# Kernel tuning notes

Measured on AMD Instinct MI355X. Metric: run time of the kernel, lower is better.

Reference implementation:

```python
import jax, jax.numpy as jnp
import numpy as np

N_NODES = 50000
N_EDGES = 800000
IN_DIM = 128
HID = 128
N_GRAPHS = 256
N_CLASSES = 2
ALPHA = 0.2  # leaky relu slope
EPS_BN = 1e-5


def setup_inputs() -> dict:
    key = jax.random.key(0)
    ks = jax.random.split(key, 24)
    adjacency = jax.random.randint(ks[0], (2, N_EDGES), 0, N_NODES, dtype=jnp.int32)
    input_feature = jax.random.normal(ks[1], (N_NODES, IN_DIM), dtype=jnp.float32)
    graph_indicator = jnp.sort(jax.random.randint(ks[2], (N_NODES,), 0, N_GRAPHS, dtype=jnp.int32))
    labels = jax.random.randint(ks[3], (N_GRAPHS,), 0, N_CLASSES, dtype=jnp.int64)
    s = 0.05
    params = {
        'W1': jax.random.normal(ks[4], (IN_DIM, HID), jnp.float32) * s,
        'a1': jax.random.normal(ks[5], (2 * HID,), jnp.float32) * s,
        'bn2_g': jnp.ones((HID,), jnp.float32),
        'bn2_b': jnp.zeros((HID,), jnp.float32),
        'W2': jax.random.normal(ks[6], (HID, HID), jnp.float32) * s,
        'a2': jax.random.normal(ks[7], (2 * HID,), jnp.float32) * s,
        'bn3_g': jnp.ones((HID,), jnp.float32),
        'bn3_b': jnp.zeros((HID,), jnp.float32),
        'W3': jax.random.normal(ks[8], (HID, HID), jnp.float32) * s,
        'a3': jax.random.normal(ks[9], (2 * HID,), jnp.float32) * s,
        'fc1_w': jax.random.normal(ks[10], (HID, 2 * HID), jnp.float32) * s,
        'fc1_b': jnp.zeros((2 * HID,), jnp.float32),
        'fc2_w': jax.random.normal(ks[11], (2 * HID, HID), jnp.float32) * s,
        'fc2_b': jnp.zeros((HID,), jnp.float32),
        'fc3_w': jax.random.normal(ks[12], (HID, N_CLASSES), jnp.float32) * s,
        'fc3_b': jnp.zeros((N_CLASSES,), jnp.float32),
    }
    return dict(adjacency=adjacency, input_feature=input_feature,
                graph_indicator=graph_indicator, labels=labels, **params)


def _batchnorm(x, g, b):
    # training-mode BatchNorm1d over node dim (biased variance)
    mu = jnp.mean(x, axis=0)
    var = jnp.mean((x - mu) ** 2, axis=0)
    return (x - mu) * jax.lax.rsqrt(var + EPS_BN) * g + b


def _sp_gat(x, src, dst, W, a):
    # pyGAT SpGraphAttentionLayer (dropout disabled / eval mode)
    h = x @ W                                # [N, F]
    F = h.shape[1]
    e_src = h @ a[:F]                        # [N]
    e_dst = h @ a[F:]                        # [N]
    e = e_src[src] + e_dst[dst]              # [E]
    ee = jnp.exp(-jax.nn.leaky_relu(e, ALPHA))
    rowsum = jax.ops.segment_sum(ee, src, num_segments=N_NODES)          # [N]
    num = jax.ops.segment_sum(ee[:, None] * h[dst], src, num_segments=N_NODES)  # [N, F]
    h_prime = num / (rowsum[:, None] + 1e-16)
    return jax.nn.elu(h_prime)


def reference(adjacency, input_feature, graph_indicator, labels,
              W1, a1, bn2_g, bn2_b, W2, a2, bn3_g, bn3_b, W3, a3,
              fc1_w, fc1_b, fc2_w, fc2_b, fc3_w, fc3_b):
    src, dst = adjacency[0], adjacency[1]
    # bn1 output is discarded in the original forward
    x = _sp_gat(input_feature, src, dst, W1, a1)
    x = _batchnorm(x, bn2_g, bn2_b)
    x = _sp_gat(x, src, dst, W2, a2)
    x = _batchnorm(x, bn3_g, bn3_b)
    x = _sp_gat(x, src, dst, W3, a3)
    # pooling_sum_4tensor: per-graph sum pooling
    pooled = jax.ops.segment_sum(x, graph_indicator, num_segments=N_GRAPHS)  # [G, F]
    x = jax.nn.relu(pooled @ fc1_w + fc1_b)
    x = jax.nn.relu(x @ fc2_w + fc2_b)
    logits = x @ fc3_w + fc3_b
    return logits
```

## Files before the change

kernel.cpp:

```cpp
#include <hip/hip_runtime.h>
#include <hip/hip_bf16.h>

#define N_NODES 50000
#define N_EDGES 800000
#define FD 128
#define N_GRAPHS 256
#define NPART 6250

typedef unsigned short u16;
typedef short bf16x8 __attribute__((ext_vector_type(8)));
typedef float f32x4 __attribute__((ext_vector_type(4)));

__device__ __forceinline__ u16 f2bf(float v) {
    __hip_bfloat16 h = __float2bfloat16(v);
    union { __hip_bfloat16 hh; u16 u; } c; c.hh = h; return c.u;
}
__device__ __forceinline__ float bf2f(u16 r) {
    return __uint_as_float(((unsigned int)r) << 16);
}

__global__ __launch_bounds__(256) void count_deg_part_k(const int* __restrict__ src,
                                                        int* __restrict__ cnt, int E) {
    int part = blockIdx.x & 7;
    int lo = part * NPART, hi = lo + NPART;
    int stride = (gridDim.x >> 3) * 256;
    for (int e = (blockIdx.x >> 3) * 256 + threadIdx.x; e < E; e += stride) {
        int s = src[e];
        if (s >= lo && s < hi) atomicAdd(&cnt[s], 1);
    }
}

__global__ __launch_bounds__(256) void fill_csr_part_k(const int* __restrict__ src,
                                                       const int* __restrict__ dst,
                                                       int* __restrict__ cur,
                                                       int* __restrict__ edst, int E) {
    int part = blockIdx.x & 7;
    int lo = part * NPART, hi = lo + NPART;
    int stride = (gridDim.x >> 3) * 256;
    for (int e = (blockIdx.x >> 3) * 256 + threadIdx.x; e < E; e += stride) {
        int s = src[e];
        if (s >= lo && s < hi) {
            int p = atomicAdd(&cur[s], 1);
            edst[p] = dst[e];
        }
    }
}

__global__ __launch_bounds__(256) void scan1_k(const int* __restrict__ cnt,
                                               int* __restrict__ bsum, int M,
                                               float* __restrict__ bnbuf,
                                               float* __restrict__ pooled) {
    int i = blockIdx.x * 256 + threadIdx.x;
    int v = (i < M) ? cnt[i] : 0;
    __shared__ int l[256];
    l[threadIdx.x] = v;
    __syncthreads();
    for (int s = 128; s > 0; s >>= 1) {
        if (threadIdx.x < s) l[threadIdx.x] += l[threadIdx.x + s];
        __syncthreads();
    }
    if (threadIdx.x == 0) bsum[blockIdx.x] = l[0];
    if (blockIdx.x == 0) {
        bnbuf[threadIdx.x] = 0.f; bnbuf[threadIdx.x + 256] = 0.f;
        for (int k = threadIdx.x; k < N_GRAPHS * FD; k += 256) pooled[k] = 0.f;
    }
}

__global__ __launch_bounds__(256) void scan3_k(const int* __restrict__ cnt,
                                               const int* __restrict__ bsum,
                                               int* __restrict__ offs,
                                               int* __restrict__ cur, int M, int NB) {
    int i = blockIdx.x * 256 + threadIdx.x;
    int tid = threadIdx.x;
    __shared__ int bs[256];
    bs[tid] = (tid < NB) ? bsum[tid] : 0;
    __syncthreads();
    for (int off = 1; off < 256; off <<= 1) {
        int t = (tid >= off) ? bs[tid - off] : 0;
        __syncthreads();
        bs[tid] += t;
        __syncthreads();
    }
    int base = (blockIdx.x == 0) ? 0 : bs[blockIdx.x - 1];
    int v = (i < M) ? cnt[i] : 0;
    __shared__ int l[256];
    l[tid] = v;
    __syncthreads();
    for (int off = 1; off < 256; off <<= 1) {
        int t = (tid >= off) ? l[tid - off] : 0;
        __syncthreads();
        l[tid] += t;
        __syncthreads();
    }
    int excl = l[tid] - v + base;
    if (i < M) { offs[i] = excl; cur[i] = excl; }
    if (i == M - 1) offs[M] = excl + v;
}

__global__ __launch_bounds__(128) void wprep1_k(const float* __restrict__ W,
                                                u16* __restrict__ Wt,
                                                float* __restrict__ cvec) {
    int n = blockIdx.x, k = threadIdx.x;
    Wt[(size_t)n * FD + k] = f2bf(W[(size_t)k * FD + n]);
    if (k == 0) cvec[n] = 0.f;
}

__global__ __launch_bounds__(128) void bnfw_k(const float* __restrict__ W,
                                              const float* __restrict__ sums,
                                              const float* __restrict__ sumsq,
                                              const float* __restrict__ g,
                                              const float* __restrict__ b,
                                              float invN,
                                              u16* __restrict__ Wt,
                                              float* __restrict__ cvec) {
    int n = blockIdx.x, k = threadIdx.x;
    __shared__ float scs[128], shs[128], l[128];
    float mu = sums[k] * invN;
    float var = sumsq[k] * invN - mu * mu;
    float sc = g[k] * rsqrtf(var + 1e-5f);
    scs[k] = sc;
    shs[k] = b[k] - mu * sc;
    __syncthreads();
    float w = W[(size_t)k * FD + n];
    Wt[(size_t)n * FD + k] = f2bf(scs[k] * w);
    l[k] = shs[k] * w;
    __syncthreads();
    for (int s = 64; s > 0; s >>= 1) {
        if (k < s) l[k] += l[k + s];
        __syncthreads();
    }
    if (k == 0) cvec[n] = l[0];
}

__global__ __launch_bounds__(256) void gemm_mfma_k(const float* __restrict__ Xf,
                                                   const u16* __restrict__ Xb,
                                                   int use_f32,
                                                   const u16* __restrict__ Wt,
                                                   const float* __restrict__ cvec,
                                                   const float* __restrict__ avec,
                                                   u16* __restrict__ Hb,
                                                   float* __restrict__ es,
                                                   float* __restrict__ ed, int M) {
    __shared__ u16 As[64][136];
    __shared__ u16 Bs[128][136];
    __shared__ float sa_s[128], sa_d[128], cv[128];
    int tid = threadIdx.x;
    if (tid < 128) { sa_s[tid] = avec[tid]; sa_d[tid] = avec[128 + tid]; cv[tid] = cvec[tid]; }
    int row0 = blockIdx.x * 64;
    {
        int n = tid >> 1, k0 = (tid & 1) * 64;
        const uint4* s = (const uint4*)(Wt + (size_t)n * FD + k0);
#pragma unroll
        for (int u = 0; u < 8; u++) *(uint4*)&Bs[n][k0 + u * 8] = s[u];
    }
    {
        int r = tid >> 2, k0 = (tid & 3) * 32;
        int grow = row0 + r;
        if (grow < M) {
            if (use_f32) {
                const float4* s = (const float4*)(Xf + (size_t)grow * FD + k0);
#pragma unroll
                for (int u = 0; u < 8; u++) {
                    float4 v = s[u];
                    ushort4 o;
                    o.x = f2bf(v.x); o.y = f2bf(v.y); o.z = f2bf(v.z); o.w = f2bf(v.w);
                    *(ushort4*)&As[r][k0 + u * 4] = o;
                }
            } else {
                const uint4* s = (const uint4*)(Xb + (size_t)grow * FD + k0);
#pragma unroll
                for (int u = 0; u < 4; u++) *(uint4*)&As[r][k0 + u * 8] = s[u];
            }
        } else {
            uint4 z = make_uint4(0, 0, 0, 0);
#pragma unroll
            for (int u = 0; u < 4; u++) *(uint4*)&As[r][k0 + u * 8] = z;
        }
    }
    __syncthreads();

    int wave = tid >> 6, lane = tid & 63;
    int quad = lane >> 4, n16 = lane & 15;
    int rbase = wave * 16;
    f32x4 acc[8];
    f32x4 zz = {0.f, 0.f, 0.f, 0.f};
#pragma unroll
    for (int t = 0; t < 8; t++) acc[t] = zz;

#pragma unroll
    for (int kk = 0; kk < 128; kk += 32) {
        bf16x8 a = *(const bf16x8*)&As[rbase + n16][kk + quad * 8];
#pragma unroll
        for (int t = 0; t < 8; t++) {
            bf16x8 b = *(const bf16x8*)&Bs[t * 16 + n16][kk + quad * 8];
            acc[t] = __builtin_amdgcn_mfma_f32_16x16x32_bf16(a, b, acc[t], 0, 0, 0);
        }
    }

#pragma unroll
    for (int reg = 0; reg < 4; reg++) {
        int grow = row0 + rbase + quad * 4 + reg;
        float vals[8];
        float ps = 0.f, pd = 0.f;
#pragma unroll
        for (int t = 0; t < 8; t++) {
            float v = acc[t][reg] + cv[t * 16 + n16];
            vals[t] = v;
            ps += v * sa_s[t * 16 + n16];
            pd += v * sa_d[t * 16 + n16];
        }
#pragma unroll
        for (int o = 8; o > 0; o >>= 1) { ps += __shfl_xor(ps, o); pd += __shfl_xor(pd, o); }
        if (grow < M) {
            if (n16 == 0) { es[grow] = ps; ed[grow] = pd; }
#pragma unroll
            for (int t = 0; t < 8; t++)
                Hb[(size_t)grow * FD + t * 16 + n16] = f2bf(vals[t]);
        }
    }
}

__global__ __launch_bounds__(256) void agg_k(const u16* __restrict__ Hb,
                                             const float* __restrict__ es_,
                                             const float* __restrict__ ed_,
                                             const int* __restrict__ offs,
                                             const int* __restrict__ edst,
                                             u16* __restrict__ Out, int M) {
    int node = __builtin_amdgcn_readfirstlane((int)((blockIdx.x * blockDim.x + threadIdx.x) >> 6));
    int lane = threadIdx.x & 63;
    if (node >= M) return;
    int s0 = offs[node], s1 = offs[node + 1];
    float esv = es_[node];
    const unsigned int* Hrow = (const unsigned int*)Hb;
    float2 a0 = make_float2(0.f, 0.f), a1 = make_float2(0.f, 0.f);
    float2 a2 = make_float2(0.f, 0.f), a3 = make_float2(0.f, 0.f);
    float rs = 0.f;
    int e = s0;
    for (; e + 8 <= s1; e += 8) {
        int d[8];
#pragma unroll
        for (int u = 0; u < 8; u++) d[u] = __builtin_amdgcn_readfirstlane(edst[e + u]);
        float w[8];
#pragma unroll
        for (int u = 0; u < 8; u++) {
            float ev = esv + ed_[d[u]];
            float lr = ev > 0.f ? ev : 0.2f * ev;
            w[u] = __expf(-lr);
        }
        unsigned int r[8];
#pragma unroll
        for (int u = 0; u < 8; u++) r[u] = Hrow[(size_t)d[u] * 64 + lane];
#pragma unroll
        for (int u = 0; u < 8; u++) {
            rs += w[u];
            float2* ac = (u & 3) == 0 ? &a0 : (u & 3) == 1 ? &a1 : (u & 3) == 2 ? &a2 : &a3;
            ac->x += w[u] * __int_as_float(r[u] << 16);
            ac->y += w[u] * __int_as_float(r[u] & 0xffff0000u);
        }
    }
    for (; e < s1; e++) {
        int d = __builtin_amdgcn_readfirstlane(edst[e]);
        float ev = esv + ed_[d];
        float lr = ev > 0.f ? ev : 0.2f * ev;
        float wv = __expf(-lr);
        rs += wv;
        unsigned int r = Hrow[(size_t)d * 64 + lane];
        a0.x += wv * __int_as_float(r << 16);
        a0.y += wv * __int_as_float(r & 0xffff0000u);
    }
    float inv = 1.f / (rs + 1e-16f);
    float vx = (a0.x + a1.x + a2.x + a3.x) * inv;
    float vy = (a0.y + a1.y + a2.y + a3.y) * inv;
    vx = vx > 0.f ? vx : (__expf(vx) - 1.f);
    vy = vy > 0.f ? vy : (__expf(vy) - 1.f);
    unsigned int pk = ((unsigned int)f2bf(vy) << 16) | f2bf(vx);
    ((unsigned int*)Out)[(size_t)node * 64 + lane] = pk;
}

__global__ void bnstats_b_k(const u16* __restrict__ Xb, float* __restrict__ sums,
                            float* __restrict__ sumsq, int M) {
    int f = threadIdx.x & 127;
    int half = threadIdx.x >> 7;
    float s1 = 0.f, s2 = 0.f;
    for (int r = blockIdx.x * 2 + half; r < M; r += gridDim.x * 2) {
        float v = bf2f(Xb[(size_t)r * FD + f]);
        s1 += v; s2 += v * v;
    }
    __shared__ float l1[256], l2[256];
    l1[threadIdx.x] = s1; l2[threadIdx.x] = s2;
    __syncthreads();
    if (half == 0) {
        atomicAdd(&sums[f], l1[f] + l1[f + 128]);
        atomicAdd(&sumsq[f], l2[f] + l2[f + 128]);
    }
}

__global__ void pool_k(const u16* __restrict__ Xb, const int* __restrict__ gi,
                       float* __restrict__ pooled, int M) {
    int f = threadIdx.x & 127;
    int half = threadIdx.x >> 7;
    int r0 = blockIdx.x * 128 + half;
    int rend = min(blockIdx.x * 128 + 128, M);
    int curg = -1; float acc = 0.f;
    for (int r = r0; r < rend; r += 2) {
        int g = gi[r];
        if (g != curg) {
            if (curg >= 0) atomicAdd(&pooled[(size_t)curg * FD + f], acc);
            curg = g; acc = 0.f;
        }
        acc += bf2f(Xb[(size_t)r * FD + f]);
    }
    if (curg >= 0) atomicAdd(&pooled[(size_t)curg * FD + f], acc);
}

__global__ __launch_bounds__(256) void mlp_k(const float* __restrict__ pooled,
                                             const float* __restrict__ fc1w, const float* __restrict__ fc1b,
                                             const float* __restrict__ fc2w, const float* __restrict__ fc2b,
                                             const float* __restrict__ fc3w, const float* __restrict__ fc3b,
                                             float* __restrict__ out) {
    int g = blockIdx.x, j = threadIdx.x;
    __shared__ float x[128], t1[256], t2[128], p0[128], p1[128];
    if (j < 128) x[j] = pooled[(size_t)g * FD + j];
    __syncthreads();
    float s = fc1b[j];
    for (int k = 0; k < 128; k++) s += x[k] * fc1w[(size_t)k * 256 + j];
    t1[j] = fmaxf(s, 0.f);
    __syncthreads();
    if (j < 128) {
        float s2 = fc2b[j];
        for (int k = 0; k < 256; k++) s2 += t1[k] * fc2w[(size_t)k * 128 + j];
        t2[j] = fmaxf(s2, 0.f);
    }
    __syncthreads();
    if (j < 128) { p0[j] = t2[j] * fc3w[j * 2]; p1[j] = t2[j] * fc3w[j * 2 + 1]; }
    __syncthreads();
    for (int s3 = 64; s3 > 0; s3 >>= 1) {
        if (j < s3) { p0[j] += p0[j + s3]; p1[j] += p1[j + s3]; }
        __syncthreads();
    }
    if (j == 0) { out[g * 2] = p0[0] + fc3b[0]; out[g * 2 + 1] = p1[0] + fc3b[1]; }
}

extern "C" void kernel_launch(void* const* d_in, const int* in_sizes, int n_in,
                              void* d_out, int out_size, void* d_ws, size_t ws_size,
                              hipStream_t stream) {
    const int*   adj  = (const int*)d_in[0];
    const float* xin  = (const float*)d_in[1];
    const int*   gi   = (const int*)d_in[2];
    const float* W1   = (const float*)d_in[4];
    const float* a1   = (const float*)d_in[5];
    const float* bn2g = (const float*)d_in[6];
    const float* bn2b = (const float*)d_in[7];
    const float* W2   = (const float*)d_in[8];
    const float* a2   = (const float*)d_in[9];
    const float* bn3g = (const float*)d_in[10];
    const float* bn3b = (const float*)d_in[11];
    const float* W3   = (const float*)d_in[12];
    const float* a3   = (const float*)d_in[13];
    const float* fc1w = (const float*)d_in[14];
    const float* fc1b = (const float*)d_in[15];
    const float* fc2w = (const float*)d_in[16];
    const float* fc2b = (const float*)d_in[17];
    const float* fc3w = (const float*)d_in[18];
    const float* fc3b = (const float*)d_in[19];
    float* out = (float*)d_out;

    const int N = N_NODES, E = N_EDGES, G = N_GRAPHS;

    u16*   Xb     = (u16*)d_ws;
    u16*   Hb     = Xb + (size_t)N * FD;
    u16*   Wt     = Hb + (size_t)N * FD;
    float* es     = (float*)(Wt + FD * FD);
    float* ed     = es + N;
    float* bnbuf  = ed + N;
    float* sumsA  = bnbuf;
    float* sumsqA = bnbuf + 128;
    float* sumsB  = bnbuf + 256;
    float* sumsqB = bnbuf + 384;
    float* cvec   = bnbuf + 512;
    float* pooled = cvec + FD;
    int*   degcnt = (int*)(pooled + (size_t)G * FD);
    int*   offs   = degcnt + N;
    int*   cur    = offs + (N + 2);
    int*   bsum   = cur + N;
    int*   edst   = bsum + 256;

    const int* srcp = adj;
    const int* dstp = adj + E;

    const int NB = (N + 255) / 256;

    hipMemsetAsync(degcnt, 0, (size_t)N * sizeof(int), stream);
    count_deg_part_k<<<8 * 392, 256, 0, stream>>>(srcp, degcnt, E);
    scan1_k<<<NB, 256, 0, stream>>>(degcnt, bsum, N, bnbuf, pooled);
    scan3_k<<<NB, 256, 0, stream>>>(degcnt, bsum, offs, cur, N, NB);
    fill_csr_part_k<<<8 * 392, 256, 0, stream>>>(srcp, dstp, cur, edst, E);

    const int gemm_grid = (N + 63) / 64;
    const int wave_grid = (N + 3) / 4;
    const float invN = 1.0f / (float)N;

    wprep1_k<<<FD, 128, 0, stream>>>(W1, Wt, cvec);
    gemm_mfma_k<<<gemm_grid, 256, 0, stream>>>(xin, Xb, 1, Wt, cvec, a1, Hb, es, ed, N);
    agg_k<<<wave_grid, 256, 0, stream>>>(Hb, es, ed, offs, edst, Xb, N);
    bnstats_b_k<<<256, 256, 0, stream>>>(Xb, sumsA, sumsqA, N);

    bnfw_k<<<FD, 128, 0, stream>>>(W2, sumsA, sumsqA, bn2g, bn2b, invN, Wt, cvec);
    gemm_mfma_k<<<gemm_grid, 256, 0, stream>>>(nullptr, Xb, 0, Wt, cvec, a2, Hb, es, ed, N);
    agg_k<<<wave_grid, 256, 0, stream>>>(Hb, es, ed, offs, edst, Xb, N);
    bnstats_b_k<<<256, 256, 0, stream>>>(Xb, sumsB, sumsqB, N);

    bnfw_k<<<FD, 128, 0, stream>>>(W3, sumsB, sumsqB, bn3g, bn3b, invN, Wt, cvec);
    gemm_mfma_k<<<gemm_grid, 256, 0, stream>>>(nullptr, Xb, 0, Wt, cvec, a3, Hb, es, ed, N);
    agg_k<<<wave_grid, 256, 0, stream>>>(Hb, es, ed, offs, edst, Xb, N);

    pool_k<<<(N + 127) / 128, 256, 0, stream>>>(Xb, gi, pooled, N);
    mlp_k<<<G, 256, 0, stream>>>(pooled, fc1w, fc1b, fc2w, fc2b, fc3w, fc3b, out);
}
```

Baseline: 428.1 us.

## Split aggregation wavefront into four edge groups with 16-byte row gathers

The per-node aggregation wavefront now splits its 64 lanes into four groups of 16. Each group gathers a different neighbor's bf16 row using 16-byte loads, so each memory instruction covers four edges instead of one. The four partial sums are combined with cross-lane shuffles before the ELU and a 16-byte store by a single group. This aims to raise memory-level parallelism and cut the instruction count of the gather, at the cost of shuffle reductions, more registers, and wasted lanes on padded tail edges.

```diff
diff --git a/kernel.cpp b/kernel.cpp
--- a/kernel.cpp
+++ b/kernel.cpp
@@ -220,6 +220,21 @@
     }
 }
 
+__device__ __forceinline__ void gat4(const uint4* __restrict__ Hq, int p, int g,
+                                     const int* d4, const float* w4, float* acc) {
+    int dg = (g & 2) ? ((g & 1) ? d4[3] : d4[2]) : ((g & 1) ? d4[1] : d4[0]);
+    float wg = (g & 2) ? ((g & 1) ? w4[3] : w4[2]) : ((g & 1) ? w4[1] : w4[0]);
+    uint4 r = Hq[(size_t)dg * 16 + p];
+    acc[0] += wg * __uint_as_float(r.x << 16);
+    acc[1] += wg * __uint_as_float(r.x & 0xffff0000u);
+    acc[2] += wg * __uint_as_float(r.y << 16);
+    acc[3] += wg * __uint_as_float(r.y & 0xffff0000u);
+    acc[4] += wg * __uint_as_float(r.z << 16);
+    acc[5] += wg * __uint_as_float(r.z & 0xffff0000u);
+    acc[6] += wg * __uint_as_float(r.w << 16);
+    acc[7] += wg * __uint_as_float(r.w & 0xffff0000u);
+}
+
 __global__ __launch_bounds__(256) void agg_k(const u16* __restrict__ Hb,
                                              const float* __restrict__ es_,
                                              const float* __restrict__ ed_,
@@ -229,52 +244,62 @@
     int node = __builtin_amdgcn_readfirstlane((int)((blockIdx.x * blockDim.x + threadIdx.x) >> 6));
     int lane = threadIdx.x & 63;
     if (node >= M) return;
+    int g = lane >> 4;
+    int p = lane & 15;
     int s0 = offs[node], s1 = offs[node + 1];
     float esv = es_[node];
-    const unsigned int* Hrow = (const unsigned int*)Hb;
-    float2 a0 = make_float2(0.f, 0.f), a1 = make_float2(0.f, 0.f);
-    float2 a2 = make_float2(0.f, 0.f), a3 = make_float2(0.f, 0.f);
+    const uint4* Hq = (const uint4*)Hb;
+    float acc[8] = {0.f, 0.f, 0.f, 0.f, 0.f, 0.f, 0.f, 0.f};
     float rs = 0.f;
     int e = s0;
     for (; e + 8 <= s1; e += 8) {
-        int d[8];
+        int d[8]; float w[8];
 #pragma unroll
         for (int u = 0; u < 8; u++) d[u] = __builtin_amdgcn_readfirstlane(edst[e + u]);
-        float w[8];
 #pragma unroll
         for (int u = 0; u < 8; u++) {
             float ev = esv + ed_[d[u]];
             float lr = ev > 0.f ? ev : 0.2f * ev;
             w[u] = __expf(-lr);
-        }
-        unsigned int r[8];
-#pragma unroll
-        for (int u = 0; u < 8; u++) r[u] = Hrow[(size_t)d[u] * 64 + lane];
-#pragma unroll
-        for (int u = 0; u < 8; u++) {
             rs += w[u];
-            float2* ac = (u & 3) == 0 ? &a0 : (u & 3) == 1 ? &a1 : (u & 3) == 2 ? &a2 : &a3;
-            ac->x += w[u] * __int_as_float(r[u] << 16);
-            ac->y += w[u] * __int_as_float(r[u] & 0xffff0000u);
-        }
-    }
-    for (; e < s1; e++) {
-        int d = __builtin_amdgcn_readfirstlane(edst[e]);
-        float ev = esv + ed_[d];
-        float lr = ev > 0.f ? ev : 0.2f * ev;
-        float wv = __expf(-lr);
-        rs += wv;
-        unsigned int r = Hrow[(size_t)d * 64 + lane];
-        a0.x += wv * __int_as_float(r << 16);
-        a0.y += wv * __int_as_float(r & 0xffff0000u);
-    }
+        }
+        gat4(Hq, p, g, d, w, acc);
+        gat4(Hq, p, g, d + 4, w + 4, acc);
+    }
+    while (e < s1) {
+        int m = s1 - e; if (m > 4) m = 4;
+        int d4[4]; float w4[4];
+#pragma unroll
+        for (int u = 0; u < 4; u++) {
+            if (u < m) {
+                int dd = __builtin_amdgcn_readfirstlane(edst[e + u]);
+                float ev = esv + ed_[dd];
+                float lr = ev > 0.f ? ev : 0.2f * ev;
+                d4[u] = dd;
+                w4[u] = __expf(-lr);
+                rs += w4[u];
+            } else { d4[u] = d4[0]; w4[u] = 0.f; }
+        }
+        gat4(Hq, p, g, d4, w4, acc);
+        e += m;
+    }
+#pragma unroll
+    for (int o = 16; o < 64; o <<= 1)
+#pragma unroll
+        for (int f = 0; f < 8; f++) acc[f] += __shfl_xor(acc[f], o);
     float inv = 1.f / (rs + 1e-16f);
-    float vx = (a0.x + a1.x + a2.x + a3.x) * inv;
-    float vy = (a0.y + a1.y + a2.y + a3.y) * inv;
-    vx = vx > 0.f ? vx : (__expf(vx) - 1.f);
-    vy = vy > 0.f ? vy : (__expf(vy) - 1.f);
-    unsigned int pk = ((unsigned int)f2bf(vy) << 16) | f2bf(vx);
-    ((unsigned int*)Out)[(size_t)node * 64 + lane] = pk;
+    if (g == 0) {
+        uint4 o4;
+        unsigned int* po = (unsigned int*)&o4;
+#pragma unroll
+        for (int q = 0; q < 4; q++) {
+            float v0 = acc[2 * q] * inv, v1 = acc[2 * q + 1] * inv;
+            v0 = v0 > 0.f ? v0 : (__expf(v0) - 1.f);
+            v1 = v1 > 0.f ? v1 : (__expf(v1) - 1.f);
+            po[q] = ((unsigned int)f2bf(v1) << 16) | f2bf(v0);
+        }
+        ((uint4*)Out)[(size_t)node * 16 + p] = o4;
+    }
 }
 
 __global__ void bnstats_b_k(const u16* __restrict__ Xb, float* __restrict__ sums,
```

New measurement: 718.2 us. +67.8%, slower.

## Gather four neighbor rows per wave with 16-byte loads in GAT aggregation

Applied to the files above, without the earlier changes.

The aggregation kernel now splits each 64-lane wave into four 16-lane groups. Each group fetches a different neighbor's 256-byte bf16 row with uint4 loads, so one wave processes four edges per load instruction instead of one. Partial sums are combined across groups with cross-lane shuffles before normalization, ELU and a vectorized store. This cuts the number of gather load instructions and raises bytes per load. The cost is extra per-edge weight computation in every lane, shuffle reductions, and only a quarter of lanes doing the final store.

```diff
diff --git a/kernel.cpp b/kernel.cpp
--- a/kernel.cpp
+++ b/kernel.cpp
@@ -220,6 +220,17 @@
     }
 }
 
+#define EW(dd) ({ float _ev = esv + ed_[dd]; float _lr = _ev > 0.f ? _ev : 0.2f * _ev; __expf(-_lr); })
+#define GACC(rr, ww) do { \
+    acc0 += (ww) * __uint_as_float((rr).x << 16); \
+    acc1 += (ww) * __uint_as_float((rr).x & 0xffff0000u); \
+    acc2 += (ww) * __uint_as_float((rr).y << 16); \
+    acc3 += (ww) * __uint_as_float((rr).y & 0xffff0000u); \
+    acc4 += (ww) * __uint_as_float((rr).z << 16); \
+    acc5 += (ww) * __uint_as_float((rr).z & 0xffff0000u); \
+    acc6 += (ww) * __uint_as_float((rr).w << 16); \
+    acc7 += (ww) * __uint_as_float((rr).w & 0xffff0000u); } while (0)
+
 __global__ __launch_bounds__(256) void agg_k(const u16* __restrict__ Hb,
                                              const float* __restrict__ es_,
                                              const float* __restrict__ ed_,
@@ -229,52 +240,80 @@
     int node = __builtin_amdgcn_readfirstlane((int)((blockIdx.x * blockDim.x + threadIdx.x) >> 6));
     int lane = threadIdx.x & 63;
     if (node >= M) return;
+    int g = lane >> 4;
+    int p = lane & 15;
     int s0 = offs[node], s1 = offs[node + 1];
     float esv = es_[node];
-    const unsigned int* Hrow = (const unsigned int*)Hb;
-    float2 a0 = make_float2(0.f, 0.f), a1 = make_float2(0.f, 0.f);
-    float2 a2 = make_float2(0.f, 0.f), a3 = make_float2(0.f, 0.f);
+    const uint4* Hq = (const uint4*)Hb;
+    float acc0 = 0.f, acc1 = 0.f, acc2 = 0.f, acc3 = 0.f;
+    float acc4 = 0.f, acc5 = 0.f, acc6 = 0.f, acc7 = 0.f;
     float rs = 0.f;
     int e = s0;
     for (; e + 8 <= s1; e += 8) {
-        int d[8];
-#pragma unroll
-        for (int u = 0; u < 8; u++) d[u] = __builtin_amdgcn_readfirstlane(edst[e + u]);
-        float w[8];
-#pragma unroll
-        for (int u = 0; u < 8; u++) {
-            float ev = esv + ed_[d[u]];
-            float lr = ev > 0.f ? ev : 0.2f * ev;
-            w[u] = __expf(-lr);
-        }
-        unsigned int r[8];
-#pragma unroll
-        for (int u = 0; u < 8; u++) r[u] = Hrow[(size_t)d[u] * 64 + lane];
-#pragma unroll
-        for (int u = 0; u < 8; u++) {
-            rs += w[u];
-            float2* ac = (u & 3) == 0 ? &a0 : (u & 3) == 1 ? &a1 : (u & 3) == 2 ? &a2 : &a3;
-            ac->x += w[u] * __int_as_float(r[u] << 16);
-            ac->y += w[u] * __int_as_float(r[u] & 0xffff0000u);
-        }
-    }
-    for (; e < s1; e++) {
-        int d = __builtin_amdgcn_readfirstlane(edst[e]);
-        float ev = esv + ed_[d];
-        float lr = ev > 0.f ? ev : 0.2f * ev;
-        float wv = __expf(-lr);
-        rs += wv;
-        unsigned int r = Hrow[(size_t)d * 64 + lane];
-        a0.x += wv * __int_as_float(r << 16);
-        a0.y += wv * __int_as_float(r & 0xffff0000u);
-    }
-    float inv = 1.f / (rs + 1e-16f);
-    float vx = (a0.x + a1.x + a2.x + a3.x) * inv;
-    float vy = (a0.y + a1.y + a2.y + a3.y) * inv;
-    vx = vx > 0.f ? vx : (__expf(vx) - 1.f);
-    vy = vy > 0.f ? vy : (__expf(vy) - 1.f);
-    unsigned int pk = ((unsigned int)f2bf(vy) << 16) | f2bf(vx);
-    ((unsigned int*)Out)[(size_t)node * 64 + lane] = pk;
+        int d0 = __builtin_amdgcn_readfirstlane(edst[e]);
+        int d1 = __builtin_amdgcn_readfirstlane(edst[e + 1]);
+        int d2 = __builtin_amdgcn_readfirstlane(edst[e + 2]);
+        int d3 = __builtin_amdgcn_readfirstlane(edst[e + 3]);
+        int d4 = __builtin_amdgcn_readfirstlane(edst[e + 4]);
+        int d5 = __builtin_amdgcn_readfirstlane(edst[e + 5]);
+        int d6 = __builtin_amdgcn_readfirstlane(edst[e + 6]);
+        int d7 = __builtin_amdgcn_readfirstlane(edst[e + 7]);
+        int dgA = g == 0 ? d0 : (g == 1 ? d1 : (g == 2 ? d2 : d3));
+        int dgB = g == 0 ? d4 : (g == 1 ? d5 : (g == 2 ? d6 : d7));
+        uint4 rA = Hq[(size_t)dgA * 16 + p];
+        uint4 rB = Hq[(size_t)dgB * 16 + p];
+        float w0 = EW(d0), w1 = EW(d1), w2 = EW(d2), w3 = EW(d3);
+        float w4 = EW(d4), w5 = EW(d5), w6 = EW(d6), w7 = EW(d7);
+        rs += w0 + w1 + w2 + w3 + w4 + w5 + w6 + w7;
+        float wgA = g == 0 ? w0 : (g == 1 ? w1 : (g == 2 ? w2 : w3));
+        float wgB = g == 0 ? w4 : (g == 1 ? w5 : (g == 2 ? w6 : w7));
+        GACC(rA, wgA);
+        GACC(rB, wgB);
+    }
+    while (e < s1) {
+        int m = s1 - e;
+        if (m > 4) m = 4;
+        int d0 = __builtin_amdgcn_readfirstlane(edst[e]);
+        int d1 = m > 1 ? __builtin_amdgcn_readfirstlane(edst[e + 1]) : d0;
+        int d2 = m > 2 ? __builtin_amdgcn_readfirstlane(edst[e + 2]) : d0;
+        int d3 = m > 3 ? __builtin_amdgcn_readfirstlane(edst[e + 3]) : d0;
+        float w0 = EW(d0);
+        float w1 = m > 1 ? EW(d1) : 0.f;
+        float w2 = m > 2 ? EW(d2) : 0.f;
+        float w3 = m > 3 ? EW(d3) : 0.f;
+        rs += w0 + w1 + w2 + w3;
+        int dgA = g == 0 ? d0 : (g == 1 ? d1 : (g == 2 ? d2 : d3));
+        float wgA = g == 0 ? w0 : (g == 1 ? w1 : (g == 2 ? w2 : w3));
+        uint4 rA = Hq[(size_t)dgA * 16 + p];
+        GACC(rA, wgA);
+        e += m;
+    }
+#pragma unroll
+    for (int o = 16; o < 64; o <<= 1) {
+        acc0 += __shfl_xor(acc0, o); acc1 += __shfl_xor(acc1, o);
+        acc2 += __shfl_xor(acc2, o); acc3 += __shfl_xor(acc3, o);
+        acc4 += __shfl_xor(acc4, o); acc5 += __shfl_xor(acc5, o);
+        acc6 += __shfl_xor(acc6, o); acc7 += __shfl_xor(acc7, o);
+    }
+    if (g == 0) {
+        float inv = 1.f / (rs + 1e-16f);
+        float v0 = acc0 * inv, v1 = acc1 * inv, v2 = acc2 * inv, v3 = acc3 * inv;
+        float v4 = acc4 * inv, v5 = acc5 * inv, v6 = acc6 * inv, v7 = acc7 * inv;
+        v0 = v0 > 0.f ? v0 : (__expf(v0) - 1.f);
+        v1 = v1 > 0.f ? v1 : (__expf(v1) - 1.f);
+        v2 = v2 > 0.f ? v2 : (__expf(v2) - 1.f);
+        v3 = v3 > 0.f ? v3 : (__expf(v3) - 1.f);
+        v4 = v4 > 0.f ? v4 : (__expf(v4) - 1.f);
+        v5 = v5 > 0.f ? v5 : (__expf(v5) - 1.f);
+        v6 = v6 > 0.f ? v6 : (__expf(v6) - 1.f);
+        v7 = v7 > 0.f ? v7 : (__expf(v7) - 1.f);
+        uint4 o4;
+        o4.x = ((unsigned int)f2bf(v1) << 16) | f2bf(v0);
+        o4.y = ((unsigned int)f2bf(v3) << 16) | f2bf(v2);
+        o4.z = ((unsigned int)f2bf(v5) << 16) | f2bf(v4);
+        o4.w = ((unsigned int)f2bf(v7) << 16) | f2bf(v6);
+        ((uint4*)Out)[(size_t)node * 16 + p] = o4;
+    }
 }
 
 __global__ void bnstats_b_k(const u16* __restrict__ Xb, float* __restrict__ sums,
```

New measurement: 433.0 us. No clear change (+1.1%).
